# Kernel tuning notes

Measured on AMD Instinct MI355X. Metric: run time of the kernel, lower is better.

## Reference

```python
import jax, jax.numpy as jnp
import numpy as np

B, E, WIN, DX, DZ, RAW = 2048, 32, 10, 14, 14, 22

def _leaky(x):
    return jnp.where(x >= 0, x, 0.01 * x)

def setup_inputs():
    key = jax.random.key(0)
    ks = jax.random.split(key, 20)
    def w(k, i, o):
        return jax.random.normal(k, (i, o), dtype=jnp.float32) / np.float32(np.sqrt(i))
    def b(k, o):
        return jax.random.normal(k, (o,), dtype=jnp.float32) * 0.01
    return {
        "raw_obs": jax.random.normal(ks[0], (B, WIN, 1, RAW), dtype=jnp.float32),
        "state_prev": jax.random.normal(ks[1], (B, E, WIN, DX), dtype=jnp.float32),
        "pm_w1": w(ks[2], WIN * DX, 256), "pm_b1": b(ks[3], 256),
        "pm_w3": w(ks[4], 256, 512), "pm_b3": b(ks[5], 512),
        "pm_wm2": w(ks[6], 512, DX), "pm_bm2": b(ks[7], DX),
        "sm_w2": w(ks[8], WIN * RAW, 256), "sm_b2": b(ks[9], 256),
        "sm_w3": w(ks[10], 256, 256), "sm_b3": b(ks[11], 256),
        "sm_w5": w(ks[12], 256, 64), "sm_b5": b(ks[13], 64),
        "sm_w6": w(ks[14], 64, DZ), "sm_b6": b(ks[15], DZ),
        "on_w1": w(ks[16], DZ, 32), "on_b1": b(ks[17], 32),
        "on_w2": w(ks[18], 32, DZ), "on_b2": b(ks[19], DZ),
    }

def reference(raw_obs, state_prev, pm_w1, pm_b1, pm_w3, pm_b3, pm_wm2, pm_bm2,
              sm_w2, sm_b2, sm_w3, sm_b3, sm_w5, sm_b5, sm_w6, sm_b6,
              on_w1, on_b1, on_w2, on_b2):
    bs, ens, win, dx = state_prev.shape
    dz = sm_w6.shape[1]
    # --- process model (LinearFlipout evaluated at mean weights) ---
    x = state_prev.reshape(bs * ens, win * dx)
    x = _leaky(x @ pm_w1 + pm_b1)
    x = _leaky(x @ pm_w3 + pm_b3)
    state_pred = (x @ pm_wm2 + pm_bm2).reshape(bs, ens, dx)   # [B,E,dx]
    state_m = state_pred.mean(axis=1)                          # [B,dx]
    A = state_pred - state_m[:, None, :]                       # [B,E,dx]
    # --- sensor model: torch repeat(E,1,1,1) tiles ensemble-major, the final
    # reshape reinterprets as batch-major; replicate that layout faithfully ---
    s = jnp.tile(raw_obs, (ens, 1, 1, 1)).reshape(bs * ens, win * raw_obs.shape[-1])
    s = _leaky(s @ sm_w2 + sm_b2)
    s = _leaky(s @ sm_w3 + sm_b3)
    s = _leaky(s @ sm_w5 + sm_b5)
    s = s @ sm_w6 + sm_b6
    ensemble_z = s.reshape(bs, ens, dz)                        # [B,E,dz]
    z = ensemble_z.mean(axis=1, keepdims=True)                 # [B,1,dz]
    # --- observation noise R = diag_embed(square(mlp(z)+c) + init) ---
    r = jax.nn.relu(z @ on_w1 + on_b1) @ on_w2 + on_b2
    r = jnp.square(r + 0.001) + 0.038729833
    R = r.reshape(bs, dz)[:, :, None] * jnp.eye(dz, dtype=r.dtype)  # [B,dz,dz]
    # --- EnKF correction ---
    S = jnp.einsum('bei,bej->bij', A, A)                       # AT @ A, [B,dx,dx]
    innovation = S / (ens - 1) + R
    K = (S / (ens - 1)) @ jnp.linalg.inv(innovation)           # [B,dx,dz]
    diff = ensemble_z - state_pred                             # (y - H_XT)^T, [B,E,dz]
    gain = jnp.einsum('bij,bej->bei', K, diff)                 # [B,E,dx]
    state_corrected = state_pred + gain
    return (state_corrected,
            state_corrected.mean(axis=1, keepdims=True),
            state_m[:, None, :],
            z,
            ensemble_z)
```

## Files before the change

kernel.cpp:

```cpp
#include <hip/hip_runtime.h>

typedef unsigned short u16;
typedef __attribute__((ext_vector_type(8))) short short8;
typedef __attribute__((ext_vector_type(4))) float floatx4;

#define MFMA_BF16 __builtin_amdgcn_mfma_f32_16x16x32_bf16

__device__ __forceinline__ u16 f2bf(float f) {
    union { float f; unsigned int i; } v; v.f = f;
    unsigned int u = v.i;
    u += 0x7fffu + ((u >> 16) & 1u);
    return (u16)(u >> 16);
}
__device__ __forceinline__ float leaky(float x) { return x >= 0.f ? x : 0.01f * x; }

#define XS 168
#define H1S 264
#define RS 232
#define H3S 72

#define O1 917504
#define O2 946176
#define O3 974848
#define O4 1003520

#define PW1   0
#define PW3   40960
#define PWM2  172032
#define PSW2  180224
#define PSW3  237568
#define PSW5  303104
#define PSW6  319488
#define PTOTAL 320512
#define WS_NEEDED 641024
#define WS_BIG (641024 + 3670016)

struct PackSeg { const float* W; int K, N, S, base, count; };
struct PackArgs { PackSeg seg[7]; };

__global__ __launch_bounds__(256) void pack_all(PackArgs pa, u16* __restrict__ P) {
    int u = blockIdx.x * 256 + threadIdx.x;
    if (u >= PTOTAL) return;
#pragma unroll
    for (int i = 0; i < 7; i++) {
        if (u >= pa.seg[i].base && u < pa.seg[i].base + pa.seg[i].count) {
            int v = u - pa.seg[i].base;
            int j = v & 7;
            int l = (v >> 3) & 63;
            int ts = v >> 9;
            int s = ts % pa.seg[i].S;
            int t = ts / pa.seg[i].S;
            int k = s * 32 + (l >> 4) * 8 + j;
            int n = t * 16 + (l & 15);
            P[u] = (k < pa.seg[i].K && n < pa.seg[i].N)
                       ? f2bf(pa.seg[i].W[k * pa.seg[i].N + n]) : (u16)0;
            return;
        }
    }
}

__global__ __launch_bounds__(256) void merged_mlp(
    const float* __restrict__ Rg, const float* __restrict__ Xg,
    const u16* __restrict__ Pk,
    const float* __restrict__ b1, const float* __restrict__ b3,
    const float* __restrict__ bm2,
    const float* __restrict__ b2, const float* __restrict__ sb3,
    const float* __restrict__ b5, const float* __restrict__ b6,
    float* __restrict__ ez_out,
    float* __restrict__ sp_ws)
{
    __shared__ __align__(16) u16 ldsA[64 * H1S];
    __shared__ __align__(16) u16 ldsB[64 * H1S];

    const int tid  = threadIdx.x;
    const int lane = tid & 63;
    const int wave = tid >> 6;
    const int q    = lane >> 4;
    const int n16  = lane & 15;

    if (blockIdx.x < 64) {
        const u16* w2p = Pk + PSW2;
        const u16* w3p = Pk + PSW3;
        const u16* w5p = Pk + PSW5;
        const u16* w6p = Pk + PSW6;
        const int row0 = blockIdx.x * 32;

        for (int idx = tid; idx < 32 * 56; idx += 256) {
            int r = idx / 56, c4 = idx - r * 56;
            float4 v = {0.f, 0.f, 0.f, 0.f};
            if (c4 < 55) v = *(const float4*)&Rg[(row0 + r) * 220 + c4 * 4];
            u16* dst = &ldsA[r * RS + c4 * 4];
            dst[0] = f2bf(v.x); dst[1] = f2bf(v.y); dst[2] = f2bf(v.z); dst[3] = f2bf(v.w);
        }
        __syncthreads();

        {
            floatx4 zero = {0.f, 0.f, 0.f, 0.f};
            floatx4 acc[2][4];
            for (int rt = 0; rt < 2; rt++)
                for (int ct = 0; ct < 4; ct++) acc[rt][ct] = zero;
#pragma unroll
            for (int s = 0; s < 7; s++) {
                short8 a0 = *(const short8*)&ldsA[n16 * RS + s * 32 + q * 8];
                short8 a1 = *(const short8*)&ldsA[(n16 + 16) * RS + s * 32 + q * 8];
#pragma unroll
                for (int ct = 0; ct < 4; ct++) {
                    int t = wave * 4 + ct;
                    short8 bf = *(const short8*)&w2p[((t * 7 + s) * 64 + lane) * 8];
                    acc[0][ct] = MFMA_BF16(a0, bf, acc[0][ct], 0, 0, 0);
                    acc[1][ct] = MFMA_BF16(a1, bf, acc[1][ct], 0, 0, 0);
                }
            }
#pragma unroll
            for (int ct = 0; ct < 4; ct++) {
                int col = (wave * 4 + ct) * 16 + n16;
                float bias = b2[col];
#pragma unroll
                for (int rt = 0; rt < 2; rt++)
#pragma unroll
                    for (int r = 0; r < 4; r++)
                        ldsB[(rt * 16 + q * 4 + r) * H1S + col] = f2bf(leaky(acc[rt][ct][r] + bias));
            }
        }
        __syncthreads();

        {
            floatx4 zero = {0.f, 0.f, 0.f, 0.f};
            floatx4 acc[2][4];
            for (int rt = 0; rt < 2; rt++)
                for (int ct = 0; ct < 4; ct++) acc[rt][ct] = zero;
#pragma unroll
            for (int s = 0; s < 8; s++) {
                short8 a0 = *(const short8*)&ldsB[n16 * H1S + s * 32 + q * 8];
                short8 a1 = *(const short8*)&ldsB[(n16 + 16) * H1S + s * 32 + q * 8];
#pragma unroll
                for (int ct = 0; ct < 4; ct++) {
                    int t = wave * 4 + ct;
                    short8 bf = *(const short8*)&w3p[((t * 8 + s) * 64 + lane) * 8];
                    acc[0][ct] = MFMA_BF16(a0, bf, acc[0][ct], 0, 0, 0);
                    acc[1][ct] = MFMA_BF16(a1, bf, acc[1][ct], 0, 0, 0);
                }
            }
#pragma unroll
            for (int ct = 0; ct < 4; ct++) {
                int col = (wave * 4 + ct) * 16 + n16;
                float bias = sb3[col];
#pragma unroll
                for (int rt = 0; rt < 2; rt++)
#pragma unroll
                    for (int r = 0; r < 4; r++)
                        ldsA[(rt * 16 + q * 4 + r) * H1S + col] = f2bf(leaky(acc[rt][ct][r] + bias));
            }
        }
        __syncthreads();

        {
            floatx4 zero = {0.f, 0.f, 0.f, 0.f};
            floatx4 acc[2] = {zero, zero};
#pragma unroll
            for (int s = 0; s < 8; s++) {
                short8 a0 = *(const short8*)&ldsA[n16 * H1S + s * 32 + q * 8];
                short8 a1 = *(const short8*)&ldsA[(n16 + 16) * H1S + s * 32 + q * 8];
                short8 bf = *(const short8*)&w5p[((wave * 8 + s) * 64 + lane) * 8];
                acc[0] = MFMA_BF16(a0, bf, acc[0], 0, 0, 0);
                acc[1] = MFMA_BF16(a1, bf, acc[1], 0, 0, 0);
            }
            int col = wave * 16 + n16;
            float bias = b5[col];
#pragma unroll
            for (int rt = 0; rt < 2; rt++)
#pragma unroll
                for (int r = 0; r < 4; r++)
                    ldsB[(rt * 16 + q * 4 + r) * H3S + col] = f2bf(leaky(acc[rt][r] + bias));
        }
        __syncthreads();

        if (wave < 2) {
            floatx4 zero = {0.f, 0.f, 0.f, 0.f};
            floatx4 acc[2] = {zero, zero};
            int s = wave;
            short8 a0 = *(const short8*)&ldsB[n16 * H3S + s * 32 + q * 8];
            short8 a1 = *(const short8*)&ldsB[(n16 + 16) * H3S + s * 32 + q * 8];
            short8 bf = *(const short8*)&w6p[(s * 64 + lane) * 8];
            acc[0] = MFMA_BF16(a0, bf, acc[0], 0, 0, 0);
            acc[1] = MFMA_BF16(a1, bf, acc[1], 0, 0, 0);
            float* pacc = (float*)ldsA;
#pragma unroll
            for (int rt = 0; rt < 2; rt++)
#pragma unroll
                for (int r = 0; r < 4; r++)
                    pacc[(wave * 32 + rt * 16 + q * 4 + r) * 16 + n16] = acc[rt][r];
        }
        __syncthreads();
        {
            const float* pacc = (const float*)ldsA;
            for (int idx = tid; idx < 512; idx += 256) {
                int r = idx >> 4, c = idx & 15;
                float v = pacc[idx] + pacc[512 + idx];
                if (c < 14) ez_out[(row0 + r) * 14 + c] = v + b6[c];
            }
        }
    } else {
        const u16* w1p  = Pk + PW1;
        const u16* w3p  = Pk + PW3;
        const u16* wm2p = Pk + PWM2;
        const int bb   = blockIdx.x - 64;
        const int row0 = bb * 64;

        for (int idx = tid; idx < 64 * 40; idx += 256) {
            int r = idx / 40, c4 = idx - r * 40;
            float4 v = {0.f, 0.f, 0.f, 0.f};
            if (c4 < 35) v = *(const float4*)&Xg[(row0 + r) * 140 + c4 * 4];
            u16* dst = &ldsA[r * XS + c4 * 4];
            dst[0] = f2bf(v.x); dst[1] = f2bf(v.y); dst[2] = f2bf(v.z); dst[3] = f2bf(v.w);
        }
        __syncthreads();

        {
            floatx4 zero = {0.f, 0.f, 0.f, 0.f};
            floatx4 acc[4][4];
            for (int rt = 0; rt < 4; rt++)
                for (int ct = 0; ct < 4; ct++) acc[rt][ct] = zero;
#pragma unroll
            for (int s = 0; s < 5; s++) {
                short8 a[4];
#pragma unroll
                for (int rt = 0; rt < 4; rt++)
                    a[rt] = *(const short8*)&ldsA[(rt * 16 + n16) * XS + s * 32 + q * 8];
#pragma unroll
                for (int ct = 0; ct < 4; ct++) {
                    int t = wave * 4 + ct;
                    short8 bf = *(const short8*)&w1p[((t * 5 + s) * 64 + lane) * 8];
#pragma unroll
                    for (int rt = 0; rt < 4; rt++)
                        acc[rt][ct] = MFMA_BF16(a[rt], bf, acc[rt][ct], 0, 0, 0);
                }
            }
#pragma unroll
            for (int ct = 0; ct < 4; ct++) {
                int col = (wave * 4 + ct) * 16 + n16;
                float bias = b1[col];
#pragma unroll
                for (int rt = 0; rt < 4; rt++)
#pragma unroll
                    for (int r = 0; r < 4; r++)
                        ldsB[(rt * 16 + q * 4 + r) * H1S + col] = f2bf(leaky(acc[rt][ct][r] + bias));
            }
        }
        __syncthreads();

        floatx4 acc3[4];
        {
            floatx4 zero = {0.f, 0.f, 0.f, 0.f};
            for (int rt = 0; rt < 4; rt++) acc3[rt] = zero;
        }
#pragma unroll
        for (int c = 0; c < 2; c++) {
            {
                floatx4 zero = {0.f, 0.f, 0.f, 0.f};
                floatx4 acc[4][4];
                for (int rt = 0; rt < 4; rt++)
                    for (int ct = 0; ct < 4; ct++) acc[rt][ct] = zero;
#pragma unroll
                for (int s = 0; s < 8; s++) {
                    short8 a[4];
#pragma unroll
                    for (int rt = 0; rt < 4; rt++)
                        a[rt] = *(const short8*)&ldsB[(rt * 16 + n16) * H1S + s * 32 + q * 8];
#pragma unroll
                    for (int ct = 0; ct < 4; ct++) {
                        int tg = c * 16 + wave * 4 + ct;
                        short8 bf = *(const short8*)&w3p[((tg * 8 + s) * 64 + lane) * 8];
#pragma unroll
                        for (int rt = 0; rt < 4; rt++)
                            acc[rt][ct] = MFMA_BF16(a[rt], bf, acc[rt][ct], 0, 0, 0);
                    }
                }
#pragma unroll
                for (int ct = 0; ct < 4; ct++) {
                    int cl = (wave * 4 + ct) * 16 + n16;
                    float bias = b3[c * 256 + cl];
#pragma unroll
                    for (int rt = 0; rt < 4; rt++)
#pragma unroll
                        for (int r = 0; r < 4; r++)
                            ldsA[(rt * 16 + q * 4 + r) * H1S + cl] = f2bf(leaky(acc[rt][ct][r] + bias));
                }
            }
            __syncthreads();
#pragma unroll
            for (int s2 = 0; s2 < 2; s2++) {
                int sl = wave * 2 + s2;
                int sg = c * 8 + sl;
                short8 bf = *(const short8*)&wm2p[(sg * 64 + lane) * 8];
#pragma unroll
                for (int rt = 0; rt < 4; rt++) {
                    short8 a = *(const short8*)&ldsA[(rt * 16 + n16) * H1S + sl * 32 + q * 8];
                    acc3[rt] = MFMA_BF16(a, bf, acc3[rt], 0, 0, 0);
                }
            }
            __syncthreads();
        }

        {
            float* pacc = (float*)ldsB;
#pragma unroll
            for (int rt = 0; rt < 4; rt++)
#pragma unroll
                for (int r = 0; r < 4; r++)
                    pacc[(wave * 64 + rt * 16 + q * 4 + r) * 16 + n16] = acc3[rt][r];
        }
        __syncthreads();
        {
            const float* pacc = (const float*)ldsB;
            for (int idx = tid; idx < 1024; idx += 256) {
                int r = idx >> 4, c = idx & 15;
                float v = pacc[idx] + pacc[1024 + idx] + pacc[2048 + idx] + pacc[3072 + idx];
                if (c < 14) sp_ws[(row0 + r) * 14 + c] = v + bm2[c];
            }
        }
    }
}

__global__ __launch_bounds__(64) void enkf_tail(
    const float* __restrict__ sp_all,
    const float* __restrict__ on_w1, const float* __restrict__ on_b1,
    const float* __restrict__ on_w2, const float* __restrict__ on_b2,
    float* out)
{
    __shared__ float spv[32][14];
    __shared__ float ezv[32][14];
    __shared__ float smv[14], zzv[14], rrv[14];
    __shared__ float M[14][14], Kmat[14][14];
    __shared__ float G[14][28];
    __shared__ float fac[14];
    __shared__ float hbuf[32];

    const int l = threadIdx.x;
    const int b = blockIdx.x;

    for (int idx = l; idx < 448; idx += 64) ((float*)spv)[idx] = sp_all[b * 448 + idx];
    {
        const float* ezsrc = out + O4 + (b & 63) * 448;
        for (int idx = l; idx < 448; idx += 64) ((float*)ezv)[idx] = ezsrc[idx];
    }

    if (l < 14) {
        float s1 = 0.f, s2 = 0.f;
        for (int e = 0; e < 32; e++) { s1 += spv[e][l]; s2 += ezv[e][l]; }
        smv[l] = s1 * (1.f / 32.f);
        zzv[l] = s2 * (1.f / 32.f);
    }
    if (l < 32) {
        float t = on_b1[l];
        for (int k = 0; k < 14; k++) t += zzv[k] * on_w1[k * 32 + l];
        hbuf[l] = t > 0.f ? t : 0.f;
    }
    if (l < 14) {
        float t = on_b2[l];
        for (int k = 0; k < 32; k++) t += hbuf[k] * on_w2[k * 14 + l];
        t += 0.001f;
        rrv[l] = t * t + 0.038729833f;
    }
    for (int idx = l; idx < 196; idx += 64) {
        int i = idx / 14, j = idx - i * 14;
        float s = 0.f;
        for (int e = 0; e < 32; e++) s += (spv[e][i] - smv[i]) * (spv[e][j] - smv[j]);
        s *= (1.f / 31.f);
        M[i][j] = s;
        G[i][j] = s + (i == j ? rrv[i] : 0.f);
        G[i][14 + j] = (i == j) ? 1.f : 0.f;
    }
    for (int c = 0; c < 14; c++) {
        float pinv = 1.f / G[c][c];
        if (l < 28) G[c][l] *= pinv;
        if (l < 14 && l != c) fac[l] = G[l][c];
        for (int idx = l; idx < 392; idx += 64) {
            int i = idx / 28, j = idx - i * 28;
            if (i != c) G[i][j] -= fac[i] * G[c][j];
        }
    }
    for (int idx = l; idx < 196; idx += 64) {
        int i = idx / 14, j = idx - i * 14;
        float s = 0.f;
        for (int k = 0; k < 14; k++) s += M[i][k] * G[k][14 + j];
        Kmat[i][j] = s;
    }
    for (int idx = l; idx < 448; idx += 64) {
        int e = idx / 14, i = idx - e * 14;
        float g = 0.f;
        for (int j = 0; j < 14; j++) g += Kmat[i][j] * (ezv[e][j] - spv[e][j]);
        out[b * 448 + idx] = spv[e][i] + g;
        out[O4 + b * 448 + idx] = ezv[e][i];
    }
    if (l < 14) {
        float g = 0.f;
        for (int j = 0; j < 14; j++) g += Kmat[l][j] * (zzv[j] - smv[j]);
        out[O1 + b * 14 + l] = smv[l] + g;
        out[O2 + b * 14 + l] = smv[l];
        out[O3 + b * 14 + l] = zzv[l];
    }
}

extern "C" void kernel_launch(void* const* d_in, const int* in_sizes, int n_in,
                              void* d_out, int out_size, void* d_ws, size_t ws_size,
                              hipStream_t stream) {
    (void)in_sizes; (void)n_in; (void)out_size; (void)ws_size;

    const float* raw_obs    = (const float*)d_in[0];
    const float* state_prev = (const float*)d_in[1];
    const float* pm_w1  = (const float*)d_in[2];
    const float* pm_b1  = (const float*)d_in[3];
    const float* pm_w3  = (const float*)d_in[4];
    const float* pm_b3  = (const float*)d_in[5];
    const float* pm_wm2 = (const float*)d_in[6];
    const float* pm_bm2 = (const float*)d_in[7];
    const float* sm_w2  = (const float*)d_in[8];
    const float* sm_b2  = (const float*)d_in[9];
    const float* sm_w3  = (const float*)d_in[10];
    const float* sm_b3  = (const float*)d_in[11];
    const float* sm_w5  = (const float*)d_in[12];
    const float* sm_b5  = (const float*)d_in[13];
    const float* sm_w6  = (const float*)d_in[14];
    const float* sm_b6  = (const float*)d_in[15];
    const float* on_w1  = (const float*)d_in[16];
    const float* on_b1  = (const float*)d_in[17];
    const float* on_w2  = (const float*)d_in[18];
    const float* on_b2  = (const float*)d_in[19];

    float* out = (float*)d_out;
    u16* P = (u16*)d_ws;
    float* sp_ws = (float*)((char*)d_ws + WS_NEEDED);

    PackArgs pa;
    pa.seg[0] = { pm_w1,  140, 256, 5,  PW1,  40960  };
    pa.seg[1] = { pm_w3,  256, 512, 8,  PW3,  131072 };
    pa.seg[2] = { pm_wm2, 512, 14,  16, PWM2, 8192   };
    pa.seg[3] = { sm_w2,  220, 256, 7,  PSW2, 57344  };
    pa.seg[4] = { sm_w3,  256, 256, 8,  PSW3, 65536  };
    pa.seg[5] = { sm_w5,  256, 64,  8,  PSW5, 16384  };
    pa.seg[6] = { sm_w6,  64,  14,  2,  PSW6, 1024   };
    pack_all<<<(PTOTAL + 255) / 256, 256, 0, stream>>>(pa, P);

    merged_mlp<<<1088, 256, 0, stream>>>(raw_obs, state_prev, P,
                                         pm_b1, pm_b3, pm_bm2,
                                         sm_b2, sm_b3, sm_b5, sm_b6,
                                         out + O4, sp_ws);
    enkf_tail<<<2048, 64, 0, stream>>>(sp_ws, on_w1, on_b1, on_w2, on_b2, out);
}
```

Measured before the change: 186.7 us.

## Shrink LDS footprint by loading X fragments directly and chunking layer three

The process-model input X is no longer staged through LDS: each wave loads float4 pieces from global memory and converts them straight into bf16 MFMA fragments, which removes one staging loop and one barrier. The 512-wide layer is now computed in four 128-column chunks into a smaller second LDS buffer, which cuts per-block shared memory and should let more blocks fit on each CU. In exchange, all four waves re-read the same X rows from global memory or cache, and the chunk loop doubles the number of barriers.

```diff
diff --git a/kernel.cpp b/kernel.cpp
--- a/kernel.cpp
+++ b/kernel.cpp
@@ -14,10 +14,10 @@
 }
 __device__ __forceinline__ float leaky(float x) { return x >= 0.f ? x : 0.01f * x; }
 
-#define XS 168
 #define H1S 264
 #define RS 232
 #define H3S 72
+#define CS 136
 
 #define O1 917504
 #define O2 946176
@@ -59,6 +59,26 @@
     }
 }
 
+__device__ __forceinline__ short8 load_x_frag(const float* __restrict__ X,
+                                              int row, int s, int q) {
+    const float* p = X + row * 140;
+    float4 v0 = {0.f, 0.f, 0.f, 0.f}, v1 = {0.f, 0.f, 0.f, 0.f};
+    int col0 = s * 32 + q * 8;
+    if (s < 4) {
+        v0 = *(const float4*)(p + col0);
+        v1 = *(const float4*)(p + col0 + 4);
+    } else {
+        if (q <= 1) v0 = *(const float4*)(p + col0);
+        if (q == 0) v1 = *(const float4*)(p + col0 + 4);
+    }
+    short8 r;
+    r[0] = (short)f2bf(v0.x); r[1] = (short)f2bf(v0.y);
+    r[2] = (short)f2bf(v0.z); r[3] = (short)f2bf(v0.w);
+    r[4] = (short)f2bf(v1.x); r[5] = (short)f2bf(v1.y);
+    r[6] = (short)f2bf(v1.z); r[7] = (short)f2bf(v1.w);
+    return r;
+}
+
 __global__ __launch_bounds__(256) void merged_mlp(
     const float* __restrict__ Rg, const float* __restrict__ Xg,
     const u16* __restrict__ Pk,
@@ -69,8 +89,8 @@
     float* __restrict__ ez_out,
     float* __restrict__ sp_ws)
 {
-    __shared__ __align__(16) u16 ldsA[64 * H1S];
-    __shared__ __align__(16) u16 ldsB[64 * H1S];
+    __shared__ __align__(16) u16 ldsH[64 * H1S];
+    __shared__ __align__(16) u16 ldsC[64 * CS];
 
     const int tid  = threadIdx.x;
     const int lane = tid & 63;
@@ -89,7 +109,7 @@
             int r = idx / 56, c4 = idx - r * 56;
             float4 v = {0.f, 0.f, 0.f, 0.f};
             if (c4 < 55) v = *(const float4*)&Rg[(row0 + r) * 220 + c4 * 4];
-            u16* dst = &ldsA[r * RS + c4 * 4];
+            u16* dst = &ldsH[r * RS + c4 * 4];
             dst[0] = f2bf(v.x); dst[1] = f2bf(v.y); dst[2] = f2bf(v.z); dst[3] = f2bf(v.w);
         }
         __syncthreads();
@@ -101,8 +121,8 @@
                 for (int ct = 0; ct < 4; ct++) acc[rt][ct] = zero;
 #pragma unroll
             for (int s = 0; s < 7; s++) {
-                short8 a0 = *(const short8*)&ldsA[n16 * RS + s * 32 + q * 8];
-                short8 a1 = *(const short8*)&ldsA[(n16 + 16) * RS + s * 32 + q * 8];
+                short8 a0 = *(const short8*)&ldsH[n16 * RS + s * 32 + q * 8];
+                short8 a1 = *(const short8*)&ldsH[(n16 + 16) * RS + s * 32 + q * 8];
 #pragma unroll
                 for (int ct = 0; ct < 4; ct++) {
                     int t = wave * 4 + ct;
@@ -119,7 +139,7 @@
                 for (int rt = 0; rt < 2; rt++)
 #pragma unroll
                     for (int r = 0; r < 4; r++)
-                        ldsB[(rt * 16 + q * 4 + r) * H1S + col] = f2bf(leaky(acc[rt][ct][r] + bias));
+                        ldsC[(rt * 16 + q * 4 + r) * H1S + col] = f2bf(leaky(acc[rt][ct][r] + bias));
             }
         }
         __syncthreads();
@@ -131,8 +151,8 @@
                 for (int ct = 0; ct < 4; ct++) acc[rt][ct] = zero;
 #pragma unroll
             for (int s = 0; s < 8; s++) {
-                short8 a0 = *(const short8*)&ldsB[n16 * H1S + s * 32 + q * 8];
-                short8 a1 = *(const short8*)&ldsB[(n16 + 16) * H1S + s * 32 + q * 8];
+                short8 a0 = *(const short8*)&ldsC[n16 * H1S + s * 32 + q * 8];
+                short8 a1 = *(const short8*)&ldsC[(n16 + 16) * H1S + s * 32 + q * 8];
 #pragma unroll
                 for (int ct = 0; ct < 4; ct++) {
                     int t = wave * 4 + ct;
@@ -149,7 +169,7 @@
                 for (int rt = 0; rt < 2; rt++)
 #pragma unroll
                     for (int r = 0; r < 4; r++)
-                        ldsA[(rt * 16 + q * 4 + r) * H1S + col] = f2bf(leaky(acc[rt][ct][r] + bias));
+                        ldsH[(rt * 16 + q * 4 + r) * H1S + col] = f2bf(leaky(acc[rt][ct][r] + bias));
             }
         }
         __syncthreads();
@@ -159,8 +179,8 @@
             floatx4 acc[2] = {zero, zero};
 #pragma unroll
             for (int s = 0; s < 8; s++) {
-                short8 a0 = *(const short8*)&ldsA[n16 * H1S + s * 32 + q * 8];
-                short8 a1 = *(const short8*)&ldsA[(n16 + 16) * H1S + s * 32 + q * 8];
+                short8 a0 = *(const short8*)&ldsH[n16 * H1S + s * 32 + q * 8];
+                short8 a1 = *(const short8*)&ldsH[(n16 + 16) * H1S + s * 32 + q * 8];
                 short8 bf = *(const short8*)&w5p[((wave * 8 + s) * 64 + lane) * 8];
                 acc[0] = MFMA_BF16(a0, bf, acc[0], 0, 0, 0);
                 acc[1] = MFMA_BF16(a1, bf, acc[1], 0, 0, 0);
@@ -171,7 +191,7 @@
             for (int rt = 0; rt < 2; rt++)
 #pragma unroll
                 for (int r = 0; r < 4; r++)
-                    ldsB[(rt * 16 + q * 4 + r) * H3S + col] = f2bf(leaky(acc[rt][r] + bias));
+                    ldsC[(rt * 16 + q * 4 + r) * H3S + col] = f2bf(leaky(acc[rt][r] + bias));
         }
         __syncthreads();
 
@@ -179,12 +199,12 @@
             floatx4 zero = {0.f, 0.f, 0.f, 0.f};
             floatx4 acc[2] = {zero, zero};
             int s = wave;
-            short8 a0 = *(const short8*)&ldsB[n16 * H3S + s * 32 + q * 8];
-            short8 a1 = *(const short8*)&ldsB[(n16 + 16) * H3S + s * 32 + q * 8];
+            short8 a0 = *(const short8*)&ldsC[n16 * H3S + s * 32 + q * 8];
+            short8 a1 = *(const short8*)&ldsC[(n16 + 16) * H3S + s * 32 + q * 8];
             short8 bf = *(const short8*)&w6p[(s * 64 + lane) * 8];
             acc[0] = MFMA_BF16(a0, bf, acc[0], 0, 0, 0);
             acc[1] = MFMA_BF16(a1, bf, acc[1], 0, 0, 0);
-            float* pacc = (float*)ldsA;
+            float* pacc = (float*)ldsH;
 #pragma unroll
             for (int rt = 0; rt < 2; rt++)
 #pragma unroll
@@ -193,7 +213,7 @@
         }
         __syncthreads();
         {
-            const float* pacc = (const float*)ldsA;
+            const float* pacc = (const float*)ldsH;
             for (int idx = tid; idx < 512; idx += 256) {
                 int r = idx >> 4, c = idx & 15;
                 float v = pacc[idx] + pacc[512 + idx];
@@ -207,15 +227,6 @@
         const int bb   = blockIdx.x - 64;
         const int row0 = bb * 64;
 
-        for (int idx = tid; idx < 64 * 40; idx += 256) {
-            int r = idx / 40, c4 = idx - r * 40;
-            float4 v = {0.f, 0.f, 0.f, 0.f};
-            if (c4 < 35) v = *(const float4*)&Xg[(row0 + r) * 140 + c4 * 4];
-            u16* dst = &ldsA[r * XS + c4 * 4];
-            dst[0] = f2bf(v.x); dst[1] = f2bf(v.y); dst[2] = f2bf(v.z); dst[3] = f2bf(v.w);
-        }
-        __syncthreads();
-
         {
             floatx4 zero = {0.f, 0.f, 0.f, 0.f};
             floatx4 acc[4][4];
@@ -226,7 +237,7 @@
                 short8 a[4];
 #pragma unroll
                 for (int rt = 0; rt < 4; rt++)
-                    a[rt] = *(const short8*)&ldsA[(rt * 16 + n16) * XS + s * 32 + q * 8];
+                    a[rt] = load_x_frag(Xg, row0 + rt * 16 + n16, s, q);
 #pragma unroll
                 for (int ct = 0; ct < 4; ct++) {
                     int t = wave * 4 + ct;
@@ -244,7 +255,7 @@
                 for (int rt = 0; rt < 4; rt++)
 #pragma unroll
                     for (int r = 0; r < 4; r++)
-                        ldsB[(rt * 16 + q * 4 + r) * H1S + col] = f2bf(leaky(acc[rt][ct][r] + bias));
+                        ldsH[(rt * 16 + q * 4 + r) * H1S + col] = f2bf(leaky(acc[rt][ct][r] + bias));
             }
         }
         __syncthreads();
@@ -255,21 +266,21 @@
             for (int rt = 0; rt < 4; rt++) acc3[rt] = zero;
         }
 #pragma unroll
-        for (int c = 0; c < 2; c++) {
+        for (int c = 0; c < 4; c++) {
             {
                 floatx4 zero = {0.f, 0.f, 0.f, 0.f};
-                floatx4 acc[4][4];
+                floatx4 acc[4][2];
                 for (int rt = 0; rt < 4; rt++)
-                    for (int ct = 0; ct < 4; ct++) acc[rt][ct] = zero;
+                    for (int ct = 0; ct < 2; ct++) acc[rt][ct] = zero;
 #pragma unroll
                 for (int s = 0; s < 8; s++) {
                     short8 a[4];
 #pragma unroll
                     for (int rt = 0; rt < 4; rt++)
-                        a[rt] = *(const short8*)&ldsB[(rt * 16 + n16) * H1S + s * 32 + q * 8];
-#pragma unroll
-                    for (int ct = 0; ct < 4; ct++) {
-                        int tg = c * 16 + wave * 4 + ct;
+                        a[rt] = *(const short8*)&ldsH[(rt * 16 + n16) * H1S + s * 32 + q * 8];
+#pragma unroll
+                    for (int ct = 0; ct < 2; ct++) {
+                        int tg = c * 8 + wave * 2 + ct;
                         short8 bf = *(const short8*)&w3p[((tg * 8 + s) * 64 + lane) * 8];
 #pragma unroll
                         for (int rt = 0; rt < 4; rt++)
@@ -277,25 +288,23 @@
                     }
                 }
 #pragma unroll
-                for (int ct = 0; ct < 4; ct++) {
-                    int cl = (wave * 4 + ct) * 16 + n16;
-                    float bias = b3[c * 256 + cl];
+                for (int ct = 0; ct < 2; ct++) {
+                    int cl = (wave * 2 + ct) * 16 + n16;
+                    float bias = b3[c * 128 + cl];
 #pragma unroll
                     for (int rt = 0; rt < 4; rt++)
 #pragma unroll
                         for (int r = 0; r < 4; r++)
-                            ldsA[(rt * 16 + q * 4 + r) * H1S + cl] = f2bf(leaky(acc[rt][ct][r] + bias));
+                            ldsC[(rt * 16 + q * 4 + r) * CS + cl] = f2bf(leaky(acc[rt][ct][r] + bias));
                 }
             }
             __syncthreads();
-#pragma unroll
-            for (int s2 = 0; s2 < 2; s2++) {
-                int sl = wave * 2 + s2;
-                int sg = c * 8 + sl;
+            {
+                int sg = c * 4 + wave;
                 short8 bf = *(const short8*)&wm2p[(sg * 64 + lane) * 8];
 #pragma unroll
                 for (int rt = 0; rt < 4; rt++) {
-                    short8 a = *(const short8*)&ldsA[(rt * 16 + n16) * H1S + sl * 32 + q * 8];
+                    short8 a = *(const short8*)&ldsC[(rt * 16 + n16) * CS + wave * 32 + q * 8];
                     acc3[rt] = MFMA_BF16(a, bf, acc3[rt], 0, 0, 0);
                 }
             }
@@ -303,7 +312,7 @@
         }
 
         {
-            float* pacc = (float*)ldsB;
+            float* pacc = (float*)ldsH;
 #pragma unroll
             for (int rt = 0; rt < 4; rt++)
 #pragma unroll
@@ -312,7 +321,7 @@
         }
         __syncthreads();
         {
-            const float* pacc = (const float*)ldsB;
+            const float* pacc = (const float*)ldsH;
             for (int idx = tid; idx < 1024; idx += 256) {
                 int r = idx >> 4, c = idx & 15;
                 float v = pacc[idx] + pacc[1024 + idx] + pacc[2048 + idx] + pacc[3072 + idx];
```

New measurement: 190.3 us. About the same (+1.9%).
